# Optimization experiments

Hardware: AMD Instinct MI355X
Metric: run time of the kernel (lower is better)

## Reference

```python
import itertools
import jax, jax.numpy as jnp
import numpy as np

B, N, C, O = 8, 32, 64, 64
PERMS = list(itertools.permutations((1, 2, 3)))  # build_idx_3_permutations order


def _lin(k, fan_in, out, lead=()):
    # torch nn.Linear default init: U(-1/sqrt(fan_in), 1/sqrt(fan_in)) for W and b
    kw, kb = jax.random.split(k)
    bound = 1.0 / float(np.sqrt(fan_in))
    W = jax.random.uniform(kw, lead + (fan_in, out), minval=-bound, maxval=bound, dtype=jnp.float32)
    b = jax.random.uniform(kb, lead + (out,), minval=-bound, maxval=bound, dtype=jnp.float32)
    return W, b


def setup_inputs() -> dict:
    key = jax.random.key(0)
    ks = jax.random.split(key, 8)
    x = jax.random.normal(ks[0], (B, N, N, N, C), dtype=jnp.float32)
    W33, b33 = _lin(ks[1], 6 * C, O)            # three_to_three linear
    W22, b22 = _lin(ks[2], 12 * C, O, (3,))     # two_to_two (a2 cat transpose), 3 diagonal planes
    W12, b12 = _lin(ks[3], 10 * C, O, (3,))     # one_to_two
    W12t, b12t = _lin(ks[4], 10 * C, O, (3,))   # one_to_two_t
    W02, b02 = _lin(ks[5], 5 * C, O, (3,))      # zero_to_two
    W11, b11 = _lin(ks[6], 10 * C, O)           # one_to_one (in_node_channels = 0)
    W01, b01 = _lin(ks[7], 5 * C, O)            # zero_to_one
    return dict(x=x, W33=W33, b33=b33, W22=W22, b22=b22, W12=W12, b12=b12,
                W12t=W12t, b12t=b12t, W02=W02, b02=b02, W11=W11, b11=b11,
                W01=W01, b01=b01)


def _contractions(x):
    """All second/first/zeroth-order mean contractions of x: [B,n,n,n,C]."""
    s1, s2, s3 = x.mean(1), x.mean(2), x.mean(3)                      # [B,n,n,C]
    # diagonals arranged as [B, other_axis, diag_axis, C]
    d12 = jnp.moveaxis(jnp.diagonal(x, axis1=1, axis2=2), -1, 2)      # [B,n3,diag,C]
    d13 = jnp.moveaxis(jnp.diagonal(x, axis1=1, axis2=3), -1, 2)      # [B,n2,diag,C]
    d23 = jnp.moveaxis(jnp.diagonal(x, axis1=2, axis2=3), -1, 2)      # [B,n1,diag,C]
    a2 = jnp.concatenate([s1, s2, s3, d12, d13, d23], axis=-1)        # [B,n,n,6C]
    tdiag = jnp.moveaxis(jnp.diagonal(d23, axis1=1, axis2=2), -1, 1)  # [B,n,C] triple diagonal x[b,i,i,i]
    a1 = jnp.concatenate([
        x.mean((1, 2)), x.mean((1, 3)), x.mean((2, 3)),               # double sums
        d12.mean(1), d12.mean(2), d13.mean(1), d13.mean(2),           # diag sums
        d23.mean(1), d23.mean(2),
        tdiag], axis=-1)                                              # [B,n,10C]
    a0 = jnp.concatenate([
        x.mean((1, 2, 3)),                                            # triple sum
        d12.mean((1, 2)), d13.mean((1, 2)), d23.mean((1, 2)),         # diag-sum-sum
        tdiag.mean(1)], axis=-1)                                      # [B,5C]
    return a2, a1, a0


def reference(x, W33, b33, W22, b22, W12, b12, W12t, b12t, W02, b02, W11, b11, W01, b01):
    n = x.shape[1]
    a2, a1, a0 = _contractions(x)
    # third-order mix: concat all 6 spatial permutations, then linear 6C -> O
    allp = jnp.concatenate([jnp.transpose(x, (0,) + p + (4,)) for p in PERMS], axis=-1)
    T = allp @ W33 + b33                                              # [B,n,n,n,O]
    # second-order mixes for the 3 diagonal planes
    a2wt = jnp.concatenate([a2, jnp.swapaxes(a2, 1, 2)], axis=-1)     # [B,n,n,12C]
    slices = []
    for i in range(3):
        m = a2wt @ W22[i] + b22[i]
        m = m + (a1 @ W12[i] + b12[i])[:, :, None, :]
        m = m + (a1 @ W12t[i] + b12t[i])[:, None, :, :]
        m = m + (a0 @ W02[i] + b02[i])[:, None, None, :]
        slices.append(m)                                              # [B,n(other),n(diag),O]
    # first-order (core-diagonal) mix
    mdiag = a1 @ W11 + b11 + (a0 @ W01 + b01)[:, None, :]             # [B,n,O]
    # _expand_mix: accumulate slices onto diagonal planes of T (diagonal_free=False)
    idx = jnp.arange(n)
    # plane (1,2): T[b,d,d,t] += slices[0][b,t,d]
    T = T.at[:, idx, idx].add(jnp.swapaxes(slices[0], 1, 2))
    # plane (1,3): T[b,d,t,d] += slices[1][b,t,d]
    Tsw = jnp.swapaxes(T, 2, 3)
    Tsw = Tsw.at[:, idx, idx].add(jnp.swapaxes(slices[1], 1, 2))
    T = jnp.swapaxes(Tsw, 2, 3)
    # plane (2,3): T[b,t,d,d] += slices[2][b,t,d]
    T = T.at[:, :, idx, idx].add(slices[2])
    # triple diagonal: T[b,d,d,d] += mdiag[b,d]
    T = T.at[:, idx, idx, idx].add(mdiag)
    return T
```

## Files before the change

kernel.cpp:

```cpp
#include <hip/hip_runtime.h>

#define NBATCH 8
#define NN 32
#define NC 64
#define NO 64
#define C6 384
#define C10 640
#define C12 768
#define C5 320

typedef __attribute__((ext_vector_type(8))) short short8;
typedef __attribute__((ext_vector_type(4))) float float4v;

static constexpr int OFF_ABF = 0;
static constexpr int OFF_A1  = 1572864;
static constexpr int OFF_A0  = 1736704;
static constexpr int OFF_R1  = 1739264;
static constexpr int OFF_R1T = 1788416;
static constexpr int OFF_R0  = 1837568;
static constexpr int OFF_MD  = 1839104;
static constexpr int OFF_WB  = 1855488;
static constexpr int OFF_WB2 = 1867776;

__device__ __forceinline__ unsigned short f2bf(float f) {
    union { float f; unsigned u; } x{f};
    unsigned r = x.u + 0x7fffu + ((x.u >> 16) & 1u);
    return (unsigned short)(r >> 16);
}

__device__ __forceinline__ void store_bf4(unsigned short* p, float4v v) {
    ushort4 w;
    w.x = f2bf(v.x); w.y = f2bf(v.y); w.z = f2bf(v.z); w.w = f2bf(v.w);
    *(ushort4*)p = w;
}

__device__ __forceinline__ float4v bf4(const unsigned short* p) {
    ushort4 u = *(const ushort4*)(p);
    float4v r;
    r.x = __uint_as_float((unsigned)u.x << 16);
    r.y = __uint_as_float((unsigned)u.y << 16);
    r.z = __uint_as_float((unsigned)u.z << 16);
    r.w = __uint_as_float((unsigned)u.w << 16);
    return r;
}

__global__ __launch_bounds__(256) void k_prep2(const float* __restrict__ W33,
                                               const float* __restrict__ W22,
                                               const float* __restrict__ x,
                                               float* __restrict__ ws) {
    if (blockIdx.x < 84) {
        int id = blockIdx.x * 256 + threadIdx.x;
        if (id < 3072) {
            int lane = id & 63;
            int ks = (id >> 6) % 12;
            int nt = (id >> 6) / 12;
            int n = nt * 16 + (lane & 15);
            int k0 = ks * 32 + (lane >> 4) * 8;
            unsigned short* dst = (unsigned short*)(ws + OFF_WB) +
                                  (size_t)((nt * 12 + ks) * 64 + lane) * 8;
#pragma unroll
            for (int jj = 0; jj < 8; ++jj) dst[jj] = f2bf(W33[(k0 + jj) * 64 + n]);
        } else if (id < 21504) {
            int q = id - 3072;
            int lane = q & 63;
            int ks = (q >> 6) % 24;
            int r = (q >> 6) / 24;
            int nt = r & 3;
            int i = r >> 2;
            int n = nt * 16 + (lane & 15);
            int k0 = ks * 32 + (lane >> 4) * 8;
            const float* W = W22 + (size_t)i * C12 * NO;
            unsigned short* dst = (unsigned short*)(ws + OFF_WB2) +
                                  (size_t)(((i * 4 + nt) * 24 + ks) * 64 + lane) * 8;
#pragma unroll
            for (int jj = 0; jj < 8; ++jj) dst[jj] = f2bf(W[(k0 + jj) * 64 + n]);
        }
        return;
    }
    int id = (blockIdx.x - 84) * 256 + threadIdx.x;
    int c4 = id & 15;
    int v = (id >> 4) & 31;
    int u = (id >> 9) & 31;
    int b = id >> 14;
    int bc = c4 * 4;
    const float* xb = x + (size_t)b * 2097152;

    float4v s1 = {0.f, 0.f, 0.f, 0.f}, s2 = s1, s3 = s1;
    {
        const float* p = xb + u * 2048 + v * 64 + bc;
        for (int i = 0; i < 32; ++i) s1 += *(const float4v*)(p + i * 65536);
    }
    {
        const float* p = xb + u * 65536 + v * 64 + bc;
        for (int j = 0; j < 32; ++j) s2 += *(const float4v*)(p + j * 2048);
    }
    {
        const float* p = xb + u * 65536 + v * 2048 + bc;
        for (int k = 0; k < 32; ++k) s3 += *(const float4v*)(p + k * 64);
    }
    float4v d12 = *(const float4v*)(xb + v * 65536 + v * 2048 + u * 64 + bc);
    float4v d13 = *(const float4v*)(xb + v * 65536 + u * 2048 + v * 64 + bc);
    float4v d23 = *(const float4v*)(xb + u * 65536 + v * 2048 + v * 64 + bc);

    const float inv = 1.0f / 32.0f;
    unsigned short* a2 = (unsigned short*)(ws + OFF_ABF) +
                         (size_t)((b * 32 + u) * 32 + v) * C6 + bc;
    store_bf4(a2 + 0 * 64, s1 * inv);
    store_bf4(a2 + 1 * 64, s2 * inv);
    store_bf4(a2 + 2 * 64, s3 * inv);
    store_bf4(a2 + 3 * 64, d12);
    store_bf4(a2 + 4 * 64, d13);
    store_bf4(a2 + 5 * 64, d23);
}

__global__ __launch_bounds__(256) void k_contract1(const float* __restrict__ x,
                                                   float* __restrict__ ws) {
    __shared__ float4v red[16][148];
    int blk = blockIdx.x;
    int b = blk >> 5;
    int t = blk & 31;
    int tid = threadIdx.x;
    int c4 = tid & 15;
    int q = tid >> 4;
    int bc = c4 * 4;
    const unsigned short* a2 = (const unsigned short*)(ws + OFF_ABF) +
                               (size_t)b * 32 * 32 * C6;

    float4v pu0 = {0.f, 0.f, 0.f, 0.f};
    float4v pu3 = pu0, pu4 = pu0, pu5 = pu0;
    float4v pv0 = pu0, pv1 = pu0, pv3 = pu0, pv4 = pu0, pv5 = pu0;
#pragma unroll
    for (int s = 0; s < 2; ++s) {
        int u = q * 2 + s;
        const unsigned short* rU = a2 + (size_t)(u * 32 + t) * C6 + bc;
        const unsigned short* rV = a2 + (size_t)(t * 32 + u) * C6 + bc;
        pu0 += bf4(rU + 0);
        pu3 += bf4(rU + 192);
        pu4 += bf4(rU + 256);
        pu5 += bf4(rU + 320);
        pv0 += bf4(rV + 0);
        pv1 += bf4(rV + 64);
        pv3 += bf4(rV + 192);
        pv4 += bf4(rV + 256);
        pv5 += bf4(rV + 320);
    }
    red[q][0 * 16 + c4] = pu0;
    red[q][1 * 16 + c4] = pv0;
    red[q][2 * 16 + c4] = pv1;
    red[q][3 * 16 + c4] = pu3;
    red[q][4 * 16 + c4] = pv3;
    red[q][5 * 16 + c4] = pu4;
    red[q][6 * 16 + c4] = pv4;
    red[q][7 * 16 + c4] = pu5;
    red[q][8 * 16 + c4] = pv5;
    __syncthreads();

    const float inv = 1.0f / 32.0f;
    float* a1 = ws + OFF_A1 + ((size_t)b * 32 + t) * C10;
    float* a0 = ws + OFF_A0 + (size_t)b * C5;
    if (tid < 144) {
        int ch = tid >> 4;
        int cc = tid & 15;
        float4v s = {0.f, 0.f, 0.f, 0.f};
#pragma unroll
        for (int qq = 0; qq < 16; ++qq) s += red[qq][ch * 16 + cc];
        s *= inv;
        *(float4v*)(a1 + ch * 64 + cc * 4) = s;
        int aidx = (ch == 0) ? 0 : (ch == 3) ? 1 : (ch == 5) ? 2 : (ch == 7) ? 3 : -1;
        if (aidx >= 0) {
#pragma unroll
            for (int e = 0; e < 4; ++e)
                atomicAdd(a0 + aidx * 64 + cc * 4 + e, s[e] * inv);
        }
    } else if (tid < 160) {
        int cc = tid - 144;
        float4v td = *(const float4v*)(x + (((size_t)b * 32 + t) * 32 + t) * 2048 +
                                       t * 64 + cc * 4);
        *(float4v*)(a1 + 9 * 64 + cc * 4) = td;
#pragma unroll
        for (int e = 0; e < 4; ++e)
            atomicAdd(a0 + 4 * 64 + cc * 4 + e, td[e] * inv);
    }
}

__global__ __launch_bounds__(256) void k_rowmix(
    const float* __restrict__ W12, const float* __restrict__ b12,
    const float* __restrict__ W12t, const float* __restrict__ b12t,
    const float* __restrict__ W02, const float* __restrict__ b02,
    const float* __restrict__ W11, const float* __restrict__ b11,
    const float* __restrict__ W01, const float* __restrict__ b01,
    float* __restrict__ ws) {
    int id = blockIdx.x * 256 + threadIdx.x;
    if (id < 98304) {
        bool second = id >= 49152;
        int q = second ? id - 49152 : id;
        int o = q & 63;
        int t = (q >> 6) & 31;
        int b = (q >> 11) & 7;
        int i = q >> 14;
        const float* W = (second ? W12t : W12) + (size_t)i * C10 * NO;
        const float* bb = (second ? b12t : b12) + i * NO;
        const float* a1 = ws + OFF_A1 + ((size_t)b * 32 + t) * C10;
        float acc = bb[o];
        for (int m = 0; m < C10; ++m) acc += a1[m] * W[m * NO + o];
        ws[(second ? OFF_R1T : OFF_R1) + (((size_t)i * 8 + b) * 32 + t) * NO + o] = acc;
    } else if (id < 114688) {
        int q = id - 98304;
        int o = q & 63;
        int t = (q >> 6) & 31;
        int b = q >> 11;
        const float* a1 = ws + OFF_A1 + ((size_t)b * 32 + t) * C10;
        const float* a0 = ws + OFF_A0 + (size_t)b * C5;
        float acc = b11[o] + b01[o];
        for (int m = 0; m < C10; ++m) acc += a1[m] * W11[m * NO + o];
        for (int m = 0; m < C5; ++m) acc += a0[m] * W01[m * NO + o];
        ws[OFF_MD + ((size_t)b * 32 + t) * NO + o] = acc;
    } else if (id < 116224) {
        int q = id - 114688;
        int o = q & 63;
        int b = (q >> 6) & 7;
        int i = q >> 9;
        const float* a0 = ws + OFF_A0 + (size_t)b * C5;
        float acc = b02[i * NO + o];
        for (int m = 0; m < C5; ++m) acc += a0[m] * W02[(size_t)i * C5 * NO + m * NO + o];
        ws[OFF_R0 + ((size_t)i * 8 + b) * NO + o] = acc;
    }
}

__global__ __launch_bounds__(256) void k_main(const float* __restrict__ x,
                                              const float* __restrict__ ws,
                                              const float* __restrict__ b33,
                                              float* __restrict__ T) {
    __shared__ __align__(16) unsigned short As[32 * 392];
    int tid = threadIdx.x;
    const unsigned short* WB = (const unsigned short*)(ws + OFF_WB);

    int wv = tid >> 6;
    int lane = tid & 63;
    int m_tile = wv & 1;
    int n_pair = wv >> 1;
    int colq = lane & 15;
    int quad = lane >> 4;

    short8 bfr[2][12];
#pragma unroll
    for (int np = 0; np < 2; ++np) {
        int nt = n_pair * 2 + np;
#pragma unroll
        for (int ks = 0; ks < 12; ++ks)
            bfr[np][ks] = *(const short8*)(WB + (size_t)((nt * 12 + ks) * 64 + lane) * 8);
    }
    float bb0 = b33[(n_pair * 2 + 0) * 16 + colq];
    float bb1 = b33[(n_pair * 2 + 1) * 16 + colq];

    int k0 = wv * 8;
    int c = colq * 4;
    int mrow = m_tile * 16 + colq;
    const unsigned short* Arow = &As[mrow * 392 + quad * 8];

    int tbase = (blockIdx.x & 7) * 1024 + (blockIdx.x >> 3) * 4;
#pragma unroll 1
    for (int r = 0; r < 4; ++r) {
        int tile = tbase + r;
        int b = tile >> 10;
        int i = (tile >> 5) & 31;
        int j = tile & 31;
        const float* xb = x + (size_t)b * 2097152;

#pragma unroll
        for (int half = 0; half < 2; ++half) {
            int k = k0 + quad + half * 4;
            float4v v0 = *(const float4v*)(xb + i * 65536 + j * 2048 + k * 64 + c);
            float4v v1 = *(const float4v*)(xb + i * 65536 + k * 2048 + j * 64 + c);
            float4v v2 = *(const float4v*)(xb + j * 65536 + i * 2048 + k * 64 + c);
            float4v v3 = *(const float4v*)(xb + k * 65536 + i * 2048 + j * 64 + c);
            float4v v4 = *(const float4v*)(xb + j * 65536 + k * 2048 + i * 64 + c);
            float4v v5 = *(const float4v*)(xb + k * 65536 + j * 2048 + i * 64 + c);
            unsigned short* dst = &As[k * 392 + c];
            store_bf4(dst + 0 * 64, v0);
            store_bf4(dst + 1 * 64, v1);
            store_bf4(dst + 2 * 64, v2);
            store_bf4(dst + 3 * 64, v3);
            store_bf4(dst + 4 * 64, v4);
            store_bf4(dst + 5 * 64, v5);
        }
        __syncthreads();

        float4v acc0 = {0.f, 0.f, 0.f, 0.f};
        float4v acc1 = {0.f, 0.f, 0.f, 0.f};
#pragma unroll
        for (int ks = 0; ks < 12; ++ks) {
            short8 a = *(const short8*)(Arow + ks * 32);
            acc0 = __builtin_amdgcn_mfma_f32_16x16x32_bf16(a, bfr[0][ks], acc0, 0, 0, 0);
            acc1 = __builtin_amdgcn_mfma_f32_16x16x32_bf16(a, bfr[1][ks], acc1, 0, 0, 0);
        }

        float* Tb = T + (size_t)tile * 2048;
#pragma unroll
        for (int rr = 0; rr < 4; ++rr) {
            int m = m_tile * 16 + quad * 4 + rr;
            int o0 = (n_pair * 2 + 0) * 16 + colq;
            int o1 = (n_pair * 2 + 1) * 16 + colq;
            __builtin_nontemporal_store(acc0[rr] + bb0, &Tb[m * 64 + o0]);
            __builtin_nontemporal_store(acc1[rr] + bb1, &Tb[m * 64 + o1]);
        }
        __syncthreads();
    }
}

__global__ __launch_bounds__(512) void k_slices(const float* __restrict__ b22,
                                                float* __restrict__ T,
                                                const float* __restrict__ ws) {
    __shared__ __align__(16) unsigned short As[32 * 776];
    int blk = blockIdx.x;
    int b = blk >> 5;
    int t = blk & 31;
    int tid = threadIdx.x;
    const unsigned short* abf = (const unsigned short*)(ws + OFF_ABF);
    const unsigned short* WB2 = (const unsigned short*)(ws + OFF_WB2);

    for (int l = tid; l < 3072; l += 512) {
        int d = l / 96;
        int m8 = l - d * 96;
        const unsigned short* src = (m8 < 48)
            ? abf + (size_t)(((b * 32 + t) * 32 + d) * C6) + m8 * 8
            : abf + (size_t)(((b * 32 + d) * 32 + t) * C6) + (m8 - 48) * 8;
        *(short8*)&As[d * 776 + m8 * 8] = *(const short8*)src;
    }
    __syncthreads();

    int wv = tid >> 6;
    int lane = tid & 63;
    int mt = wv & 1;
    int nt = wv >> 1;
    float4v zero = {0.f, 0.f, 0.f, 0.f};
    float4v acc[3] = {zero, zero, zero};
    const unsigned short* Arow = &As[(mt * 16 + (lane & 15)) * 776 + (lane >> 4) * 8];
#pragma unroll
    for (int ks = 0; ks < 24; ++ks) {
        short8 a = *(const short8*)(Arow + ks * 32);
#pragma unroll
        for (int i = 0; i < 3; ++i) {
            short8 bf = *(const short8*)(WB2 + (size_t)(((i * 4 + nt) * 24 + ks) * 64 + lane) * 8);
            acc[i] = __builtin_amdgcn_mfma_f32_16x16x32_bf16(a, bf, acc[i], 0, 0, 0);
        }
    }

    int colq = lane & 15;
    int quad = lane >> 4;
    float* Tb = T + (size_t)b * 2097152;
    int o = nt * 16 + colq;
    float base0 = b22[0 * 64 + o] + ws[OFF_R1 + ((size_t)(0 * 8 + b) * 32 + t) * 64 + o]
                + ws[OFF_R0 + (size_t)(0 * 8 + b) * 64 + o];
    float base1 = b22[1 * 64 + o] + ws[OFF_R1 + ((size_t)(1 * 8 + b) * 32 + t) * 64 + o]
                + ws[OFF_R0 + (size_t)(1 * 8 + b) * 64 + o];
    float base2 = b22[2 * 64 + o] + ws[OFF_R1 + ((size_t)(2 * 8 + b) * 32 + t) * 64 + o]
                + ws[OFF_R0 + (size_t)(2 * 8 + b) * 64 + o];
#pragma unroll
    for (int r = 0; r < 4; ++r) {
        int d = mt * 16 + quad * 4 + r;
        float s0 = acc[0][r] + base0 + ws[OFF_R1T + ((size_t)(0 * 8 + b) * 32 + d) * 64 + o];
        float s1 = acc[1][r] + base1 + ws[OFF_R1T + ((size_t)(1 * 8 + b) * 32 + d) * 64 + o];
        float s2 = acc[2][r] + base2 + ws[OFF_R1T + ((size_t)(2 * 8 + b) * 32 + d) * 64 + o];
        if (d != t) {
            Tb[d * 65536 + d * 2048 + t * 64 + o] += s0;
            Tb[d * 65536 + t * 2048 + d * 64 + o] += s1;
            Tb[t * 65536 + d * 2048 + d * 64 + o] += s2;
        } else {
            float md = ws[OFF_MD + ((size_t)b * 32 + d) * 64 + o];
            Tb[d * 65536 + d * 2048 + d * 64 + o] += s0 + s1 + s2 + md;
        }
    }
}

extern "C" void kernel_launch(void* const* d_in, const int* in_sizes, int n_in,
                              void* d_out, int out_size, void* d_ws, size_t ws_size,
                              hipStream_t stream) {
    const float* x    = (const float*)d_in[0];
    const float* W33  = (const float*)d_in[1];
    const float* b33  = (const float*)d_in[2];
    const float* W22  = (const float*)d_in[3];
    const float* b22  = (const float*)d_in[4];
    const float* W12  = (const float*)d_in[5];
    const float* b12  = (const float*)d_in[6];
    const float* W12t = (const float*)d_in[7];
    const float* b12t = (const float*)d_in[8];
    const float* W02  = (const float*)d_in[9];
    const float* b02  = (const float*)d_in[10];
    const float* W11  = (const float*)d_in[11];
    const float* b11  = (const float*)d_in[12];
    const float* W01  = (const float*)d_in[13];
    const float* b01  = (const float*)d_in[14];
    float* T  = (float*)d_out;
    float* ws = (float*)d_ws;

    hipMemsetAsync(ws + OFF_A0, 0, (size_t)NBATCH * C5 * sizeof(float), stream);
    hipLaunchKernelGGL(k_prep2, dim3(596), dim3(256), 0, stream, W33, W22, x, ws);
    hipLaunchKernelGGL(k_contract1, dim3(256), dim3(256), 0, stream, x, ws);
    hipLaunchKernelGGL(k_rowmix, dim3(454), dim3(256), 0, stream,
                       W12, b12, W12t, b12t, W02, b02, W11, b11, W01, b01, ws);
    hipLaunchKernelGGL(k_main, dim3(2048), dim3(256), 0, stream, x, ws, b33, T);
    hipLaunchKernelGGL(k_slices, dim3(256), dim3(512), 0, stream, b22, T, ws);
}
```

Measured before the change: 249.1 us.

## Stage bf16 copy of x during contraction pass and use it in main GEMM

The prep kernel now writes a bf16 copy of x into workspace while it computes the s3 reduction, and the main kernel gathers its six permuted operands from that half-size copy instead of re-reading fp32 x and converting. This is meant to halve the gather traffic in the dominant kernel. The main kernel also changes from four tiles per block to one tile per block, launching 8192 blocks. In exchange it adds 32 MB of extra writes in prep, and the bf16 path only runs when the workspace is large enough; otherwise the fp32 path is used.

```diff
diff --git a/kernel.cpp b/kernel.cpp
--- a/kernel.cpp
+++ b/kernel.cpp
@@ -21,6 +21,8 @@
 static constexpr int OFF_MD  = 1839104;
 static constexpr int OFF_WB  = 1855488;
 static constexpr int OFF_WB2 = 1867776;
+static constexpr int OFF_XBF = 1941504;
+static constexpr size_t NEED_XBF_FLOATS = (size_t)1941504 + 8388608;
 
 __device__ __forceinline__ unsigned short f2bf(float f) {
     union { float f; unsigned u; } x{f};
@@ -44,6 +46,7 @@
     return r;
 }
 
+template <bool WX>
 __global__ __launch_bounds__(256) void k_prep2(const float* __restrict__ W33,
                                                const float* __restrict__ W22,
                                                const float* __restrict__ x,
@@ -95,8 +98,14 @@
         for (int j = 0; j < 32; ++j) s2 += *(const float4v*)(p + j * 2048);
     }
     {
+        unsigned short* xbf = (unsigned short*)(ws + OFF_XBF) +
+                              (size_t)b * 2097152 + u * 65536 + v * 2048 + bc;
         const float* p = xb + u * 65536 + v * 2048 + bc;
-        for (int k = 0; k < 32; ++k) s3 += *(const float4v*)(p + k * 64);
+        for (int k = 0; k < 32; ++k) {
+            float4v xv = *(const float4v*)(p + k * 64);
+            s3 += xv;
+            if (WX) store_bf4(xbf + k * 64, xv);
+        }
     }
     float4v d12 = *(const float4v*)(xb + v * 65536 + v * 2048 + u * 64 + bc);
     float4v d13 = *(const float4v*)(xb + v * 65536 + u * 2048 + v * 64 + bc);
@@ -227,6 +236,7 @@
     }
 }
 
+template <bool BFX>
 __global__ __launch_bounds__(256) void k_main(const float* __restrict__ x,
                                               const float* __restrict__ ws,
                                               const float* __restrict__ b33,
@@ -258,15 +268,33 @@
     int mrow = m_tile * 16 + colq;
     const unsigned short* Arow = &As[mrow * 392 + quad * 8];
 
-    int tbase = (blockIdx.x & 7) * 1024 + (blockIdx.x >> 3) * 4;
-#pragma unroll 1
-    for (int r = 0; r < 4; ++r) {
-        int tile = tbase + r;
-        int b = tile >> 10;
-        int i = (tile >> 5) & 31;
-        int j = tile & 31;
+    int tile = (blockIdx.x & 7) * 1024 + (blockIdx.x >> 3);
+    int b = tile >> 10;
+    int i = (tile >> 5) & 31;
+    int j = tile & 31;
+
+    if (BFX) {
+        const unsigned short* xs = (const unsigned short*)(ws + OFF_XBF) +
+                                   (size_t)b * 2097152;
+#pragma unroll
+        for (int half = 0; half < 2; ++half) {
+            int k = k0 + quad + half * 4;
+            ushort4 v0 = *(const ushort4*)(xs + i * 65536 + j * 2048 + k * 64 + c);
+            ushort4 v1 = *(const ushort4*)(xs + i * 65536 + k * 2048 + j * 64 + c);
+            ushort4 v2 = *(const ushort4*)(xs + j * 65536 + i * 2048 + k * 64 + c);
+            ushort4 v3 = *(const ushort4*)(xs + k * 65536 + i * 2048 + j * 64 + c);
+            ushort4 v4 = *(const ushort4*)(xs + j * 65536 + k * 2048 + i * 64 + c);
+            ushort4 v5 = *(const ushort4*)(xs + k * 65536 + j * 2048 + i * 64 + c);
+            unsigned short* dst = &As[k * 392 + c];
+            *(ushort4*)(dst + 0 * 64) = v0;
+            *(ushort4*)(dst + 1 * 64) = v1;
+            *(ushort4*)(dst + 2 * 64) = v2;
+            *(ushort4*)(dst + 3 * 64) = v3;
+            *(ushort4*)(dst + 4 * 64) = v4;
+            *(ushort4*)(dst + 5 * 64) = v5;
+        }
+    } else {
         const float* xb = x + (size_t)b * 2097152;
-
 #pragma unroll
         for (int half = 0; half < 2; ++half) {
             int k = k0 + quad + half * 4;
@@ -284,27 +312,26 @@
             store_bf4(dst + 4 * 64, v4);
             store_bf4(dst + 5 * 64, v5);
         }
-        __syncthreads();
-
-        float4v acc0 = {0.f, 0.f, 0.f, 0.f};
-        float4v acc1 = {0.f, 0.f, 0.f, 0.f};
-#pragma unroll
-        for (int ks = 0; ks < 12; ++ks) {
-            short8 a = *(const short8*)(Arow + ks * 32);
-            acc0 = __builtin_amdgcn_mfma_f32_16x16x32_bf16(a, bfr[0][ks], acc0, 0, 0, 0);
-            acc1 = __builtin_amdgcn_mfma_f32_16x16x32_bf16(a, bfr[1][ks], acc1, 0, 0, 0);
-        }
-
-        float* Tb = T + (size_t)tile * 2048;
-#pragma unroll
-        for (int rr = 0; rr < 4; ++rr) {
-            int m = m_tile * 16 + quad * 4 + rr;
-            int o0 = (n_pair * 2 + 0) * 16 + colq;
-            int o1 = (n_pair * 2 + 1) * 16 + colq;
-            __builtin_nontemporal_store(acc0[rr] + bb0, &Tb[m * 64 + o0]);
-            __builtin_nontemporal_store(acc1[rr] + bb1, &Tb[m * 64 + o1]);
-        }
-        __syncthreads();
+    }
+    __syncthreads();
+
+    float4v acc0 = {0.f, 0.f, 0.f, 0.f};
+    float4v acc1 = {0.f, 0.f, 0.f, 0.f};
+#pragma unroll
+    for (int ks = 0; ks < 12; ++ks) {
+        short8 a = *(const short8*)(Arow + ks * 32);
+        acc0 = __builtin_amdgcn_mfma_f32_16x16x32_bf16(a, bfr[0][ks], acc0, 0, 0, 0);
+        acc1 = __builtin_amdgcn_mfma_f32_16x16x32_bf16(a, bfr[1][ks], acc1, 0, 0, 0);
+    }
+
+    float* Tb = T + (size_t)tile * 2048;
+#pragma unroll
+    for (int rr = 0; rr < 4; ++rr) {
+        int m = m_tile * 16 + quad * 4 + rr;
+        int o0 = (n_pair * 2 + 0) * 16 + colq;
+        int o1 = (n_pair * 2 + 1) * 16 + colq;
+        __builtin_nontemporal_store(acc0[rr] + bb0, &Tb[m * 64 + o0]);
+        __builtin_nontemporal_store(acc1[rr] + bb1, &Tb[m * 64 + o1]);
     }
 }
 
@@ -394,11 +421,21 @@
     float* T  = (float*)d_out;
     float* ws = (float*)d_ws;
 
+    const bool bfx = ws_size >= NEED_XBF_FLOATS * sizeof(float);
+
     hipMemsetAsync(ws + OFF_A0, 0, (size_t)NBATCH * C5 * sizeof(float), stream);
-    hipLaunchKernelGGL(k_prep2, dim3(596), dim3(256), 0, stream, W33, W22, x, ws);
+    if (bfx) {
+        hipLaunchKernelGGL(k_prep2<true>, dim3(596), dim3(256), 0, stream, W33, W22, x, ws);
+    } else {
+        hipLaunchKernelGGL(k_prep2<false>, dim3(596), dim3(256), 0, stream, W33, W22, x, ws);
+    }
     hipLaunchKernelGGL(k_contract1, dim3(256), dim3(256), 0, stream, x, ws);
     hipLaunchKernelGGL(k_rowmix, dim3(454), dim3(256), 0, stream,
                        W12, b12, W12t, b12t, W02, b02, W11, b11, W01, b01, ws);
-    hipLaunchKernelGGL(k_main, dim3(2048), dim3(256), 0, stream, x, ws, b33, T);
+    if (bfx) {
+        hipLaunchKernelGGL(k_main<true>, dim3(8192), dim3(256), 0, stream, x, ws, b33, T);
+    } else {
+        hipLaunchKernelGGL(k_main<false>, dim3(8192), dim3(256), 0, stream, x, ws, b33, T);
+    }
     hipLaunchKernelGGL(k_slices, dim3(256), dim3(512), 0, stream, b22, T, ws);
 }
```

Result: slower. 269.2 us (+8.1%).
